# Optimization experiments

Measured on AMD Instinct MI355X. Metric: run time of the kernel, lower is better.

The kernel has to match this reference:

```python
import jax, jax.numpy as jnp
import numpy as np

B, S, D, H = 1, 2048, 1024, 16
HD = D // H  # head_dim = 64
ROPE_BASE = 10000.0


def setup_inputs() -> dict:
    key = jax.random.key(0)
    k1, k2, k3, k4, k5 = jax.random.split(key, 5)
    std = 0.02
    return {
        "hidden_states": jax.random.normal(k1, (B, S, D), dtype=jnp.float32),
        "attention_mask": jnp.ones((B, S), dtype=jnp.int32),
        "position_ids": jnp.broadcast_to(jnp.arange(S, dtype=jnp.int32), (B, S)),
        "wq": jax.random.normal(k2, (D, D), dtype=jnp.float32) * std,
        "wk": jax.random.normal(k3, (D, D), dtype=jnp.float32) * std,
        "wv": jax.random.normal(k4, (D, D), dtype=jnp.float32) * std,
        "wo": jax.random.normal(k5, (D, D), dtype=jnp.float32) * std,
    }


def _rope_cos_sin(position_ids):
    # standard llama freqs: 1/base^(2i/hd), interleaved-pair rotation
    inv_freq = 1.0 / (ROPE_BASE ** (jnp.arange(0, HD, 2, dtype=jnp.float32) / HD))  # [HD/2]
    freqs = position_ids.astype(jnp.float32)[..., None] * inv_freq  # [B,S,HD/2]
    # add head axis for broadcasting: [B,S,1,HD/2]
    return jnp.cos(freqs)[:, :, None, :], jnp.sin(freqs)[:, :, None, :]


def _apply_rope(x, cos, sin):
    # x: [B,S,H,HD]; pairs (x0,x1) rotated as complex (x0+i*x1)*(cos+i*sin)
    x2 = x.reshape(x.shape[:-1] + (HD // 2, 2))
    x0, x1 = x2[..., 0], x2[..., 1]
    out = jnp.stack([x0 * cos - x1 * sin, x0 * sin + x1 * cos], axis=-1)
    return out.reshape(x.shape)


def _attention(hidden_states, attention_mask, position_ids, wq, wk, wv, wo):
    xq = (hidden_states @ wq).reshape(B, S, H, HD)
    xk = (hidden_states @ wk).reshape(B, S, H, HD)
    xv = (hidden_states @ wv).reshape(B, S, H, HD)

    cos, sin = _rope_cos_sin(position_ids)
    xq = _apply_rope(xq, cos, sin)
    xk = _apply_rope(xk, cos, sin)

    # combined causal + padding mask -> additive bias
    causal = jnp.tril(jnp.ones((S, S), dtype=bool))[None, None]  # [1,1,S,S]
    pad = (attention_mask > 0)[:, None, None, :]  # [B,1,1,S]
    mask = jnp.logical_and(causal, pad)
    neg = jnp.finfo(jnp.float32).min
    bias = jnp.where(mask, 0.0, neg).astype(jnp.float32)

    scale = 1.0 / np.sqrt(HD).astype(np.float32)
    scores = jnp.einsum("bqhd,bkhd->bhqk", xq, xk) * scale + bias  # [B,H,S,S]
    attn_weights = jax.nn.softmax(scores, axis=-1)

    attn_output = jnp.einsum("bhqk,bkhd->bqhd", attn_weights, xv)
    attn_output = attn_output.reshape(B, S, D)
    return attn_output @ wo


def reference(hidden_states, attention_mask, position_ids, wq, wk, wv, wo):
    return _attention(hidden_states, attention_mask, position_ids, wq, wk, wv, wo)
```

## Files before the change

kernel.cpp:

```cpp
#include <hip/hip_runtime.h>
#include <stdint.h>

#define SEQ 2048
#define DMODEL 1024
#define NHEAD 16
#define HDIM 64
#define KCH 256
#define NCH 8
#define NIT32 288

typedef unsigned short u16;
typedef __attribute__((ext_vector_type(4))) float f32x4;
typedef __attribute__((ext_vector_type(8))) __bf16 bf16x8;
typedef __attribute__((ext_vector_type(8))) u16 u16x8;

__device__ __forceinline__ u16 f2bf(float f) {
  unsigned int u = __builtin_bit_cast(unsigned int, f);
  unsigned int r = (u + 0x7FFFu + ((u >> 16) & 1u)) >> 16;
  return (u16)r;
}
__device__ __forceinline__ float bf2f(u16 b) {
  unsigned int u = ((unsigned int)b) << 16;
  return __builtin_bit_cast(float, u);
}
__device__ __forceinline__ bf16x8 load8(const u16* p) {
  return __builtin_bit_cast(bf16x8, *(const u16x8*)p);
}
__device__ __forceinline__ void gl_lds16(const void* g, void* l) {
  __builtin_amdgcn_global_load_lds(
      (const __attribute__((address_space(1))) unsigned int*)g,
      (__attribute__((address_space(3))) unsigned int*)l, 16, 0, 0);
}

__global__ __launch_bounds__(256) void convert_x(const float* __restrict__ X,
                                                 u16* __restrict__ Xb) {
  int i = (blockIdx.x * 256 + threadIdx.x) * 4;
  float4 v = *(const float4*)(X + i);
  union { u16 s[4]; uint2 u; } o;
  o.s[0] = f2bf(v.x); o.s[1] = f2bf(v.y); o.s[2] = f2bf(v.z); o.s[3] = f2bf(v.w);
  *(uint2*)(Xb + i) = o.u;
}

__global__ __launch_bounds__(256) void transpose_w(
    const float* __restrict__ W0, const float* __restrict__ W1,
    const float* __restrict__ W2, const float* __restrict__ W3,
    u16* __restrict__ T0, u16* __restrict__ T1,
    u16* __restrict__ T2, u16* __restrict__ T3) {
  __shared__ u16 tile[64][65];
  int bz = blockIdx.z;
  const float* W = bz == 0 ? W0 : bz == 1 ? W1 : bz == 2 ? W2 : W3;
  u16* T = bz == 0 ? T0 : bz == 1 ? T1 : bz == 2 ? T2 : T3;
  int n0 = blockIdx.x * 64, k0 = blockIdx.y * 64;
  int t = threadIdx.x;
#pragma unroll 4
  for (int i = 0; i < 16; ++i) {
    int idx = i * 256 + t;
    int r = idx >> 6, c = idx & 63;
    tile[r][c] = f2bf(W[(k0 + r) * 1024 + n0 + c]);
  }
  __syncthreads();
#pragma unroll 4
  for (int i = 0; i < 16; ++i) {
    int idx = i * 256 + t;
    int r = idx >> 6, c = idx & 63;
    T[(n0 + r) * 1024 + k0 + c] = tile[c][r];
  }
}

template <int BM, int BN, int NMATS, bool OUTF32>
__global__ __launch_bounds__(256) void gemm_bf16(
    const u16* __restrict__ A, const u16* __restrict__ B0,
    const u16* __restrict__ B1, const u16* __restrict__ B2,
    u16* __restrict__ O0, u16* __restrict__ O1, u16* __restrict__ O2,
    float* __restrict__ OF) {
  constexpr int MI = BM / 32, NI = BN / 32;
  constexpr int LA = BM / 64, LB = BN / 64;
  __shared__ u16 As[BM * 32];
  __shared__ u16 Bs[BN * 32];
  const int t = threadIdx.x;
  const int lane = t & 63, w = t >> 6;
  const int g = lane >> 4, li = lane & 15;
  const int n0g = blockIdx.x * BN;
  const int mat = n0g >> 10;
  const int n0 = n0g & 1023;
  const u16* Bp = (NMATS == 1 || mat == 0) ? B0 : (mat == 1 ? B1 : B2);
  const int m0 = blockIdx.y * BM;
  const int wm = (w >> 1) * (BM / 2), wn = (w & 1) * (BN / 2);
  f32x4 acc[MI][NI] = {};
  for (int k0 = 0; k0 < 1024; k0 += 32) {
#pragma unroll
    for (int it = 0; it < LA; ++it) {
      int L = it * 2048 + t * 8;
      int r = L >> 5, c = L & 31;
      gl_lds16(A + (m0 + r) * 1024 + k0 + c, (char*)As + it * 4096 + w * 1024);
    }
#pragma unroll
    for (int it = 0; it < LB; ++it) {
      int L = it * 2048 + t * 8;
      int r = L >> 5, c = L & 31;
      gl_lds16(Bp + (n0 + r) * 1024 + k0 + c, (char*)Bs + it * 4096 + w * 1024);
    }
    __syncthreads();
    bf16x8 af[MI], bfr[NI];
#pragma unroll
    for (int mi = 0; mi < MI; ++mi) af[mi] = load8(&As[(wm + mi * 16 + li) * 32 + g * 8]);
#pragma unroll
    for (int ni = 0; ni < NI; ++ni) bfr[ni] = load8(&Bs[(wn + ni * 16 + li) * 32 + g * 8]);
#pragma unroll
    for (int mi = 0; mi < MI; ++mi)
#pragma unroll
      for (int ni = 0; ni < NI; ++ni)
        acc[mi][ni] = __builtin_amdgcn_mfma_f32_16x16x32_bf16(af[mi], bfr[ni], acc[mi][ni], 0, 0, 0);
    __syncthreads();
  }
  u16* Ob = (NMATS == 1 || mat == 0) ? O0 : (mat == 1 ? O1 : O2);
#pragma unroll
  for (int mi = 0; mi < MI; ++mi)
#pragma unroll
    for (int ni = 0; ni < NI; ++ni)
#pragma unroll
      for (int r = 0; r < 4; ++r) {
        int m = m0 + wm + mi * 16 + g * 4 + r;
        int n = n0 + wn + ni * 16 + li;
        float v = acc[mi][ni][r];
        if (OUTF32) OF[m * 1024 + n] = v;
        else Ob[m * 1024 + n] = f2bf(v);
      }
}

__global__ __launch_bounds__(256) void rope_qk(u16* __restrict__ Qb, u16* __restrict__ Kb,
                                               const int* __restrict__ pos_ids) {
  int gid = blockIdx.x * 256 + threadIdx.x;
  int s = gid >> 9;
  int rem = gid & 511;
  int h = rem >> 5, i = rem & 31;
  float pos = (float)pos_ids[s];
  float inv = exp2f(-(float)i * (13.287712379549449f / 32.0f));
  float ang = pos * inv;
  float sn, cs;
  sincosf(ang, &sn, &cs);
  int base = s * 1024 + h * 64 + 2 * i;
  {
    float x0 = bf2f(Qb[base]), x1 = bf2f(Qb[base + 1]);
    Qb[base]     = f2bf((x0 * cs - x1 * sn) * 0.125f);
    Qb[base + 1] = f2bf((x0 * sn + x1 * cs) * 0.125f);
  }
  {
    float x0 = bf2f(Kb[base]), x1 = bf2f(Kb[base + 1]);
    Kb[base]     = f2bf(x0 * cs - x1 * sn);
    Kb[base + 1] = f2bf(x0 * sn + x1 * cs);
  }
}

__global__ __launch_bounds__(256) void v_transpose(const u16* __restrict__ Vb,
                                                   u16* __restrict__ Vt) {
  __shared__ u16 tile[64][65];
  const int t = threadIdx.x;
  const int s0 = blockIdx.x * 64, h = blockIdx.y;
#pragma unroll 4
  for (int i = 0; i < 16; ++i) {
    int idx = i * 256 + t;
    int r = idx >> 6, c = idx & 63;
    tile[r][c] = Vb[(s0 + r) * 1024 + h * 64 + c];
  }
  __syncthreads();
#pragma unroll 4
  for (int i = 0; i < 16; ++i) {
    int idx = i * 256 + t;
    int d = idx >> 6, sc = idx & 63;
    Vt[h * (64 * 2048) + d * 2048 + s0 + sc] = tile[sc][d];
  }
}

__global__ __launch_bounds__(256) void attn_partial(
    const u16* __restrict__ Qb, const u16* __restrict__ Kb,
    const u16* __restrict__ Vt, const int* __restrict__ amask,
    float* __restrict__ Mpart, float* __restrict__ Lpart, u16* __restrict__ Opart) {
  const int t = threadIdx.x, lane = t & 63, w = t >> 6;
  const int g = lane >> 4, li = lane & 15;
  const int bid = blockIdx.x;
  const int h = bid & 15;
  const int j = (bid >> 4) * 4 + w;
  __shared__ u16 Plds[4][2][16][72];
  const u16* Vh = Vt + h * (64 * 2048);
  const int c = (j >= 280) ? 7 : (j >= 264) ? 6 : (j >= 240) ? 5 : (j >= 208) ? 4
              : (j >= 168) ? 3 : (j >= 120) ? 2 : (j >= 64) ? 1 : 0;
  const int qb = 8 * c + (j - (64 * c - 4 * c * (c - 1)));
  const int q0 = qb * 32;
  const int kstart = c * KCH;
  const int kend = min(kstart + KCH, q0 + 32);
  bf16x8 qf[2][2];
#pragma unroll
  for (int a = 0; a < 2; ++a)
#pragma unroll
    for (int hf = 0; hf < 2; ++hf)
      qf[a][hf] = load8(Qb + (q0 + a * 16 + li) * 1024 + h * 64 + hf * 32 + g * 8);
  f32x4 acc[2][4] = {};
  float mrow[2][4], lrow[2][4];
#pragma unroll
  for (int a = 0; a < 2; ++a)
#pragma unroll
    for (int r = 0; r < 4; ++r) { mrow[a][r] = -1e30f; lrow[a][r] = 0.f; }
  for (int k0 = kstart; k0 < kend; k0 += 64) {
    f32x4 sc[2][4] = {};
#pragma unroll
    for (int s = 0; s < 4; ++s) {
      bf16x8 kf0 = load8(Kb + (k0 + s * 16 + li) * 1024 + h * 64 + 0 + g * 8);
      bf16x8 kf1 = load8(Kb + (k0 + s * 16 + li) * 1024 + h * 64 + 32 + g * 8);
#pragma unroll
      for (int a = 0; a < 2; ++a) {
        sc[a][s] = __builtin_amdgcn_mfma_f32_16x16x32_bf16(qf[a][0], kf0, sc[a][s], 0, 0, 0);
        sc[a][s] = __builtin_amdgcn_mfma_f32_16x16x32_bf16(qf[a][1], kf1, sc[a][s], 0, 0, 0);
      }
    }
    float sv[2][4][4];
    float tmax[2][4];
#pragma unroll
    for (int a = 0; a < 2; ++a)
#pragma unroll
      for (int r = 0; r < 4; ++r) tmax[a][r] = -1e30f;
#pragma unroll
    for (int s = 0; s < 4; ++s) {
      int key = k0 + s * 16 + li;
      bool kok = (amask[key] != 0);
#pragma unroll
      for (int a = 0; a < 2; ++a)
#pragma unroll
        for (int r = 0; r < 4; ++r) {
          int q = q0 + a * 16 + g * 4 + r;
          float v = (kok && key <= q) ? sc[a][s][r] : -1e30f;
          sv[a][s][r] = v;
          tmax[a][r] = fmaxf(tmax[a][r], v);
        }
    }
#pragma unroll
    for (int m = 1; m < 16; m <<= 1)
#pragma unroll
      for (int a = 0; a < 2; ++a)
#pragma unroll
        for (int r = 0; r < 4; ++r)
          tmax[a][r] = fmaxf(tmax[a][r], __shfl_xor(tmax[a][r], m, 64));
    float alpha[2][4];
#pragma unroll
    for (int a = 0; a < 2; ++a)
#pragma unroll
      for (int r = 0; r < 4; ++r) {
        float mn = fmaxf(mrow[a][r], tmax[a][r]);
        alpha[a][r] = __expf(mrow[a][r] - mn);
        mrow[a][r] = mn;
      }
    float ps[2][4] = {};
#pragma unroll
    for (int s = 0; s < 4; ++s)
#pragma unroll
      for (int a = 0; a < 2; ++a)
#pragma unroll
        for (int r = 0; r < 4; ++r) {
          float p = __expf(sv[a][s][r] - mrow[a][r]);
          ps[a][r] += p;
          Plds[w][a][g * 4 + r][s * 16 + li] = f2bf(p);
        }
#pragma unroll
    for (int m = 1; m < 16; m <<= 1)
#pragma unroll
      for (int a = 0; a < 2; ++a)
#pragma unroll
        for (int r = 0; r < 4; ++r) ps[a][r] += __shfl_xor(ps[a][r], m, 64);
#pragma unroll
    for (int a = 0; a < 2; ++a)
#pragma unroll
      for (int r = 0; r < 4; ++r) lrow[a][r] = lrow[a][r] * alpha[a][r] + ps[a][r];
#pragma unroll
    for (int a = 0; a < 2; ++a)
#pragma unroll
      for (int ti = 0; ti < 4; ++ti)
#pragma unroll
        for (int r = 0; r < 4; ++r) acc[a][ti][r] *= alpha[a][r];
    bf16x8 pf[2][2];
#pragma unroll
    for (int a = 0; a < 2; ++a)
#pragma unroll
      for (int ks = 0; ks < 2; ++ks)
        pf[a][ks] = load8(&Plds[w][a][li][ks * 32 + g * 8]);
#pragma unroll
    for (int ti = 0; ti < 4; ++ti) {
      bf16x8 vf0 = load8(Vh + (ti * 16 + li) * 2048 + k0 + 0 + g * 8);
      bf16x8 vf1 = load8(Vh + (ti * 16 + li) * 2048 + k0 + 32 + g * 8);
#pragma unroll
      for (int a = 0; a < 2; ++a) {
        acc[a][ti] = __builtin_amdgcn_mfma_f32_16x16x32_bf16(pf[a][0], vf0, acc[a][ti], 0, 0, 0);
        acc[a][ti] = __builtin_amdgcn_mfma_f32_16x16x32_bf16(pf[a][1], vf1, acc[a][ti], 0, 0, 0);
      }
    }
  }
  const int idx = (h * 64 + qb) * NCH + c;
  if (li == 0) {
#pragma unroll
    for (int a = 0; a < 2; ++a)
#pragma unroll
      for (int r = 0; r < 4; ++r) {
        Mpart[idx * 32 + a * 16 + g * 4 + r] = mrow[a][r];
        Lpart[idx * 32 + a * 16 + g * 4 + r] = lrow[a][r];
      }
  }
#pragma unroll
  for (int a = 0; a < 2; ++a)
#pragma unroll
    for (int ti = 0; ti < 4; ++ti)
#pragma unroll
      for (int r = 0; r < 4; ++r)
        Opart[idx * 2048 + (a * 16 + g * 4 + r) * 64 + ti * 16 + li] = f2bf(acc[a][ti][r]);
}

__global__ __launch_bounds__(256) void attn_combine(
    const float* __restrict__ Mpart, const float* __restrict__ Lpart,
    const u16* __restrict__ Opart, u16* __restrict__ Ab) {
  const int qb = blockIdx.x, h = blockIdx.y;
  const int t = threadIdx.x;
  const int q = t >> 3, dg = t & 7;
  const int nch = qb / 8 + 1;
  const int base = (h * 64 + qb) * NCH;
  float M = -1e30f;
#pragma unroll
  for (int c = 0; c < NCH; ++c)
    if (c < nch) M = fmaxf(M, Mpart[(base + c) * 32 + q]);
  float L = 0.f;
  float o[8] = {};
#pragma unroll
  for (int c = 0; c < NCH; ++c)
    if (c < nch) {
      float e = __expf(Mpart[(base + c) * 32 + q] - M);
      L += e * Lpart[(base + c) * 32 + q];
      uint4 pk = *(const uint4*)(Opart + (base + c) * 2048 + q * 64 + dg * 8);
      const u16* ps = (const u16*)&pk;
#pragma unroll
      for (int jj = 0; jj < 8; ++jj) o[jj] += e * bf2f(ps[jj]);
    }
  float inv = 1.f / L;
  u16* dst = Ab + (qb * 32 + q) * 1024 + h * 64 + dg * 8;
  union { u16 s[8]; uint4 u; } ou;
#pragma unroll
  for (int jj = 0; jj < 8; ++jj) ou.s[jj] = f2bf(o[jj] * inv);
  *(uint4*)dst = ou.u;
}

extern "C" void kernel_launch(void* const* d_in, const int* in_sizes, int n_in,
                              void* d_out, int out_size, void* d_ws, size_t ws_size,
                              hipStream_t stream) {
  const float* X = (const float*)d_in[0];
  const int* amask = (const int*)d_in[1];
  const int* pos = (const int*)d_in[2];
  const float* wq = (const float*)d_in[3];
  const float* wk = (const float*)d_in[4];
  const float* wv = (const float*)d_in[5];
  const float* wo = (const float*)d_in[6];
  float* out = (float*)d_out;
  char* ws = (char*)d_ws;
  u16* Xb  = (u16*)(ws);
  u16* Wtq = (u16*)(ws + (4u  << 20));
  u16* Wtk = (u16*)(ws + (6u  << 20));
  u16* Wtv = (u16*)(ws + (8u  << 20));
  u16* Wto = (u16*)(ws + (10u << 20));
  u16* Qb  = (u16*)(ws + (12u << 20));
  u16* Kb  = (u16*)(ws + (16u << 20));
  u16* Vb  = (u16*)(ws + (20u << 20));
  u16* Vt  = (u16*)(ws + (24u << 20));
  u16* Ab  = (u16*)(ws + (28u << 20));
  float* Mpart = (float*)(ws + (32u << 20));
  float* Lpart = (float*)(ws + (33u << 20));
  u16*   Opart = (u16*)(ws + (34u << 20));

  convert_x<<<2048, 256, 0, stream>>>(X, Xb);
  transpose_w<<<dim3(16, 16, 4), 256, 0, stream>>>(wq, wk, wv, wo, Wtq, Wtk, Wtv, Wto);
  gemm_bf16<64, 128, 3, false><<<dim3(24, 32), 256, 0, stream>>>(Xb, Wtq, Wtk, Wtv, Qb, Kb, Vb, nullptr);
  rope_qk<<<4096, 256, 0, stream>>>(Qb, Kb, pos);
  v_transpose<<<dim3(32, 16), 256, 0, stream>>>(Vb, Vt);
  attn_partial<<<1152, 256, 0, stream>>>(Qb, Kb, Vt, amask, Mpart, Lpart, Opart);
  attn_combine<<<dim3(64, 16), 256, 0, stream>>>(Mpart, Lpart, Opart, Ab);
  gemm_bf16<64, 64, 1, true><<<dim3(16, 32), 256, 0, stream>>>(Ab, Wto, nullptr, nullptr,
                                                               nullptr, nullptr, nullptr, out);
}
```

Baseline: 117.2 us.

## Rewrite attention partial kernel with 32x32 MFMA, register-only P and exp2 softmax

Restructures the flash-attention partial kernel to use 32x32x16 bf16 MFMA with transposed scores (K as A operand), so each lane owns one query column and row reductions become a single cross-half shuffle. The P matrix is repacked into MFMA operand layout with lane shuffles instead of an LDS round trip. Masking is skipped for fully unmasked off-diagonal key tiles via a ballot, and log2(e) is folded into the Q scale so softmax uses exp2. The key step shrinks to 32, which means more loop iterations, and the new shuffle-based repacking must be exactly right for the output to stay correct.

```diff
diff --git a/kernel.cpp b/kernel.cpp
--- a/kernel.cpp
+++ b/kernel.cpp
@@ -7,10 +7,10 @@
 #define HDIM 64
 #define KCH 256
 #define NCH 8
-#define NIT32 288
 
 typedef unsigned short u16;
 typedef __attribute__((ext_vector_type(4))) float f32x4;
+typedef __attribute__((ext_vector_type(16))) float f32x16;
 typedef __attribute__((ext_vector_type(8))) __bf16 bf16x8;
 typedef __attribute__((ext_vector_type(8))) u16 u16x8;
 
@@ -140,10 +140,11 @@
   float sn, cs;
   sincosf(ang, &sn, &cs);
   int base = s * 1024 + h * 64 + 2 * i;
+  const float qs = 0.125f * 1.4426950408889634f;
   {
     float x0 = bf2f(Qb[base]), x1 = bf2f(Qb[base + 1]);
-    Qb[base]     = f2bf((x0 * cs - x1 * sn) * 0.125f);
-    Qb[base + 1] = f2bf((x0 * sn + x1 * cs) * 0.125f);
+    Qb[base]     = f2bf((x0 * cs - x1 * sn) * qs);
+    Qb[base + 1] = f2bf((x0 * sn + x1 * cs) * qs);
   }
   {
     float x0 = bf2f(Kb[base]), x1 = bf2f(Kb[base + 1]);
@@ -177,139 +178,107 @@
     const u16* __restrict__ Vt, const int* __restrict__ amask,
     float* __restrict__ Mpart, float* __restrict__ Lpart, u16* __restrict__ Opart) {
   const int t = threadIdx.x, lane = t & 63, w = t >> 6;
-  const int g = lane >> 4, li = lane & 15;
+  const int l31 = lane & 31;
+  const int hi = lane >> 5;
+  const int hi4 = hi * 4;
   const int bid = blockIdx.x;
   const int h = bid & 15;
   const int j = (bid >> 4) * 4 + w;
-  __shared__ u16 Plds[4][2][16][72];
-  const u16* Vh = Vt + h * (64 * 2048);
   const int c = (j >= 280) ? 7 : (j >= 264) ? 6 : (j >= 240) ? 5 : (j >= 208) ? 4
               : (j >= 168) ? 3 : (j >= 120) ? 2 : (j >= 64) ? 1 : 0;
   const int qb = 8 * c + (j - (64 * c - 4 * c * (c - 1)));
   const int q0 = qb * 32;
   const int kstart = c * KCH;
   const int kend = min(kstart + KCH, q0 + 32);
-  bf16x8 qf[2][2];
-#pragma unroll
-  for (int a = 0; a < 2; ++a)
-#pragma unroll
-    for (int hf = 0; hf < 2; ++hf)
-      qf[a][hf] = load8(Qb + (q0 + a * 16 + li) * 1024 + h * 64 + hf * 32 + g * 8);
-  f32x4 acc[2][4] = {};
-  float mrow[2][4], lrow[2][4];
-#pragma unroll
-  for (int a = 0; a < 2; ++a)
-#pragma unroll
-    for (int r = 0; r < 4; ++r) { mrow[a][r] = -1e30f; lrow[a][r] = 0.f; }
-  for (int k0 = kstart; k0 < kend; k0 += 64) {
-    f32x4 sc[2][4] = {};
-#pragma unroll
-    for (int s = 0; s < 4; ++s) {
-      bf16x8 kf0 = load8(Kb + (k0 + s * 16 + li) * 1024 + h * 64 + 0 + g * 8);
-      bf16x8 kf1 = load8(Kb + (k0 + s * 16 + li) * 1024 + h * 64 + 32 + g * 8);
-#pragma unroll
-      for (int a = 0; a < 2; ++a) {
-        sc[a][s] = __builtin_amdgcn_mfma_f32_16x16x32_bf16(qf[a][0], kf0, sc[a][s], 0, 0, 0);
-        sc[a][s] = __builtin_amdgcn_mfma_f32_16x16x32_bf16(qf[a][1], kf1, sc[a][s], 0, 0, 0);
+  const u16* Vh = Vt + h * (64 * 2048);
+  bf16x8 qf[4];
+#pragma unroll
+  for (int d16 = 0; d16 < 4; ++d16)
+    qf[d16] = load8(Qb + (q0 + l31) * 1024 + h * 64 + d16 * 16 + hi * 8);
+  f32x16 acc0 = {}, acc1 = {};
+  float m = -1e30f, lsum = 0.f;
+  for (int k0 = kstart; k0 < kend; k0 += 32) {
+    unsigned int kmsk = (unsigned int)__ballot(amask[k0 + l31] != 0);
+    f32x16 s = {};
+#pragma unroll
+    for (int d16 = 0; d16 < 4; ++d16) {
+      bf16x8 kf = load8(Kb + (k0 + l31) * 1024 + h * 64 + d16 * 16 + hi * 8);
+      s = __builtin_amdgcn_mfma_f32_32x32x16_bf16(kf, qf[d16], s, 0, 0, 0);
+    }
+    float sv[16];
+    float tmax = -1e30f;
+    if (k0 < q0 && kmsk == 0xFFFFFFFFu) {
+#pragma unroll
+      for (int i = 0; i < 16; ++i) { sv[i] = s[i]; tmax = fmaxf(tmax, s[i]); }
+    } else {
+      const int qrel = q0 + l31 - k0 - hi4;
+      const unsigned int mk = kmsk >> hi4;
+#pragma unroll
+      for (int i = 0; i < 16; ++i) {
+        const int koff = (i & 3) + 8 * (i >> 2);
+        bool ok = (((mk >> koff) & 1u) != 0u) && (koff <= qrel);
+        float v = ok ? s[i] : -1e30f;
+        sv[i] = v;
+        tmax = fmaxf(tmax, v);
       }
     }
-    float sv[2][4][4];
-    float tmax[2][4];
-#pragma unroll
-    for (int a = 0; a < 2; ++a)
-#pragma unroll
-      for (int r = 0; r < 4; ++r) tmax[a][r] = -1e30f;
-#pragma unroll
-    for (int s = 0; s < 4; ++s) {
-      int key = k0 + s * 16 + li;
-      bool kok = (amask[key] != 0);
-#pragma unroll
-      for (int a = 0; a < 2; ++a)
-#pragma unroll
-        for (int r = 0; r < 4; ++r) {
-          int q = q0 + a * 16 + g * 4 + r;
-          float v = (kok && key <= q) ? sc[a][s][r] : -1e30f;
-          sv[a][s][r] = v;
-          tmax[a][r] = fmaxf(tmax[a][r], v);
-        }
-    }
-#pragma unroll
-    for (int m = 1; m < 16; m <<= 1)
-#pragma unroll
-      for (int a = 0; a < 2; ++a)
-#pragma unroll
-        for (int r = 0; r < 4; ++r)
-          tmax[a][r] = fmaxf(tmax[a][r], __shfl_xor(tmax[a][r], m, 64));
-    float alpha[2][4];
-#pragma unroll
-    for (int a = 0; a < 2; ++a)
-#pragma unroll
-      for (int r = 0; r < 4; ++r) {
-        float mn = fmaxf(mrow[a][r], tmax[a][r]);
-        alpha[a][r] = __expf(mrow[a][r] - mn);
-        mrow[a][r] = mn;
-      }
-    float ps[2][4] = {};
-#pragma unroll
-    for (int s = 0; s < 4; ++s)
-#pragma unroll
-      for (int a = 0; a < 2; ++a)
-#pragma unroll
-        for (int r = 0; r < 4; ++r) {
-          float p = __expf(sv[a][s][r] - mrow[a][r]);
-          ps[a][r] += p;
-          Plds[w][a][g * 4 + r][s * 16 + li] = f2bf(p);
-        }
-#pragma unroll
-    for (int m = 1; m < 16; m <<= 1)
-#pragma unroll
-      for (int a = 0; a < 2; ++a)
-#pragma unroll
-        for (int r = 0; r < 4; ++r) ps[a][r] += __shfl_xor(ps[a][r], m, 64);
-#pragma unroll
-    for (int a = 0; a < 2; ++a)
-#pragma unroll
-      for (int r = 0; r < 4; ++r) lrow[a][r] = lrow[a][r] * alpha[a][r] + ps[a][r];
-#pragma unroll
-    for (int a = 0; a < 2; ++a)
-#pragma unroll
-      for (int ti = 0; ti < 4; ++ti)
-#pragma unroll
-        for (int r = 0; r < 4; ++r) acc[a][ti][r] *= alpha[a][r];
-    bf16x8 pf[2][2];
-#pragma unroll
-    for (int a = 0; a < 2; ++a)
-#pragma unroll
-      for (int ks = 0; ks < 2; ++ks)
-        pf[a][ks] = load8(&Plds[w][a][li][ks * 32 + g * 8]);
-#pragma unroll
-    for (int ti = 0; ti < 4; ++ti) {
-      bf16x8 vf0 = load8(Vh + (ti * 16 + li) * 2048 + k0 + 0 + g * 8);
-      bf16x8 vf1 = load8(Vh + (ti * 16 + li) * 2048 + k0 + 32 + g * 8);
-#pragma unroll
-      for (int a = 0; a < 2; ++a) {
-        acc[a][ti] = __builtin_amdgcn_mfma_f32_16x16x32_bf16(pf[a][0], vf0, acc[a][ti], 0, 0, 0);
-        acc[a][ti] = __builtin_amdgcn_mfma_f32_16x16x32_bf16(pf[a][1], vf1, acc[a][ti], 0, 0, 0);
-      }
+    float pmax = fmaxf(tmax, __shfl_xor(tmax, 32, 64));
+    float mn = fmaxf(m, pmax);
+    float alpha = exp2f(m - mn);
+    m = mn;
+    float p[16];
+    float ps = 0.f;
+#pragma unroll
+    for (int i = 0; i < 16; ++i) { p[i] = exp2f(sv[i] - mn); ps += p[i]; }
+    ps += __shfl_xor(ps, 32, 64);
+    lsum = lsum * alpha + ps;
+    acc0 *= alpha;
+    acc1 *= alpha;
+    unsigned int pk[8], ot[8];
+#pragma unroll
+    for (int jj = 0; jj < 8; ++jj)
+      pk[jj] = (unsigned int)f2bf(p[2 * jj]) | ((unsigned int)f2bf(p[2 * jj + 1]) << 16);
+#pragma unroll
+    for (int jj = 0; jj < 8; ++jj) ot[jj] = __shfl_xor(pk[jj], 32, 64);
+    union { unsigned int u[4]; bf16x8 v; } f1, f2;
+    f1.u[0] = hi ? ot[2] : pk[0];
+    f1.u[1] = hi ? ot[3] : pk[1];
+    f1.u[2] = hi ? pk[2] : ot[0];
+    f1.u[3] = hi ? pk[3] : ot[1];
+    f2.u[0] = hi ? ot[6] : pk[4];
+    f2.u[1] = hi ? ot[7] : pk[5];
+    f2.u[2] = hi ? pk[6] : ot[4];
+    f2.u[3] = hi ? pk[7] : ot[5];
+    {
+      bf16x8 va = load8(Vh + (0 + l31) * 2048 + k0 + hi * 8);
+      bf16x8 vb = load8(Vh + (0 + l31) * 2048 + k0 + 16 + hi * 8);
+      acc0 = __builtin_amdgcn_mfma_f32_32x32x16_bf16(va, f1.v, acc0, 0, 0, 0);
+      acc0 = __builtin_amdgcn_mfma_f32_32x32x16_bf16(vb, f2.v, acc0, 0, 0, 0);
+    }
+    {
+      bf16x8 va = load8(Vh + (32 + l31) * 2048 + k0 + hi * 8);
+      bf16x8 vb = load8(Vh + (32 + l31) * 2048 + k0 + 16 + hi * 8);
+      acc1 = __builtin_amdgcn_mfma_f32_32x32x16_bf16(va, f1.v, acc1, 0, 0, 0);
+      acc1 = __builtin_amdgcn_mfma_f32_32x32x16_bf16(vb, f2.v, acc1, 0, 0, 0);
     }
   }
   const int idx = (h * 64 + qb) * NCH + c;
-  if (li == 0) {
-#pragma unroll
-    for (int a = 0; a < 2; ++a)
-#pragma unroll
-      for (int r = 0; r < 4; ++r) {
-        Mpart[idx * 32 + a * 16 + g * 4 + r] = mrow[a][r];
-        Lpart[idx * 32 + a * 16 + g * 4 + r] = lrow[a][r];
-      }
-  }
-#pragma unroll
-  for (int a = 0; a < 2; ++a)
-#pragma unroll
-    for (int ti = 0; ti < 4; ++ti)
-#pragma unroll
-      for (int r = 0; r < 4; ++r)
-        Opart[idx * 2048 + (a * 16 + g * 4 + r) * 64 + ti * 16 + li] = f2bf(acc[a][ti][r]);
+  if (hi == 0) {
+    Mpart[idx * 32 + l31] = m;
+    Lpart[idx * 32 + l31] = lsum;
+  }
+  u16* outp = Opart + idx * 2048 + l31 * 64;
+#pragma unroll
+  for (int grp = 0; grp < 4; ++grp) {
+    union { u16 s4[4]; uint2 u; } o0, o1;
+#pragma unroll
+    for (int r = 0; r < 4; ++r) {
+      o0.s4[r] = f2bf(acc0[grp * 4 + r]);
+      o1.s4[r] = f2bf(acc1[grp * 4 + r]);
+    }
+    *(uint2*)(outp + grp * 8 + hi4) = o0.u;
+    *(uint2*)(outp + 32 + grp * 8 + hi4) = o1.u;
+  }
 }
 
 __global__ __launch_bounds__(256) void attn_combine(
@@ -329,7 +298,7 @@
 #pragma unroll
   for (int c = 0; c < NCH; ++c)
     if (c < nch) {
-      float e = __expf(Mpart[(base + c) * 32 + q] - M);
+      float e = exp2f(Mpart[(base + c) * 32 + q] - M);
       L += e * Lpart[(base + c) * 32 + q];
       uint4 pk = *(const uint4*)(Opart + (base + c) * 2048 + q * 64 + dg * 8);
       const u16* ps = (const u16*)&pk;
```

Measured after the change: 120.0 us. +2.3%, slower.
